# Kernel optimization log

Measured on AMD Instinct MI355X. Metric: run time of the kernel, lower is better.

Reference implementation:

```python
import jax, jax.numpy as jnp
import numpy as np
from jax import lax

B, S, DIMS, T, K = 4, 4096, 2048, 10, 2


def setup_inputs() -> dict:
    key = jax.random.key(0)
    ks = jax.random.split(key, 4)
    scale = 1.0 / np.sqrt(DIMS)
    x = jax.random.normal(ks[0], (B, S, DIMS), dtype=jnp.float32)
    W_cls = jax.random.normal(ks[1], (DIMS, T), dtype=jnp.float32) * scale
    W_sparse = jax.random.normal(ks[2], (DIMS, T), dtype=jnp.float32) * scale
    W_gates = jax.random.normal(ks[3], (DIMS, T), dtype=jnp.float32) * scale
    return {
        "x": x,
        "W_cls": W_cls, "b_cls": jnp.zeros((T,), jnp.float32),
        "W_sparse": W_sparse, "b_sparse": jnp.zeros((T,), jnp.float32),
        "W_gates": W_gates, "b_gates": jnp.zeros((T,), jnp.float32),
        "alpha": jnp.ones((1,), jnp.float32),
    }


def reference(x, W_cls, b_cls, W_sparse, b_sparse, W_gates, b_gates, alpha):
    # soft routing: softmax classifier over num_types
    soft_types = jax.nn.softmax(jnp.einsum("bsd,dt->bst", x, W_cls) + b_cls, axis=-1)
    # sparse routing: top-k over logits, softmax over the k kept logits,
    # scattered back into a dense [B,S,T] gate vector (zeros elsewhere)
    logits = jnp.einsum("bsd,dt->bst", x, W_sparse) + b_sparse
    top_v, top_i = lax.top_k(logits, K)                      # [B,S,K]
    sparse_g = jax.nn.softmax(top_v, axis=-1)                # [B,S,K]
    # scatter via one-hot (K and T are tiny)
    sparse_types = jnp.sum(jax.nn.one_hot(top_i, T, dtype=x.dtype) * sparse_g[..., None], axis=-2)  # [B,S,T]
    # per-type sigmoid gates: batched single matmul == stack of Linear(dims,1)+Sigmoid
    gates = jax.nn.sigmoid(jnp.einsum("bsd,dt->bst", x, W_gates) + b_gates)  # [B,S,T]
    a = jax.nn.sigmoid(alpha)                                # [1], broadcasts
    mixed_types = a * sparse_types + (1.0 - a) * soft_types  # [B,S,T]
    # original: gates stacked as [B,S,1,T], mixed unsqueezed to [B,S,1,T], sum over T -> [B,S,1]
    return jnp.sum(gates * mixed_types, axis=-1, keepdims=True)
```

## Files before the change

### kernel.cpp

```cpp
#include <hip/hip_runtime.h>
#include <math.h>
#include <stdint.h>


#define NROWS   16384
#define DIMS_   2048
#define TT      10
#define PIPE_D  3

typedef __attribute__((ext_vector_type(8))) short short8;
typedef __attribute__((ext_vector_type(4))) float f32x4;

__device__ __forceinline__ unsigned short bf16_rne(float f) {
    unsigned int u = __float_as_uint(f);
    unsigned int r = u + 0x7fffu + ((u >> 16) & 1u);
    return (unsigned short)(r >> 16);
}

__global__ __launch_bounds__(256)
void tgate_k0(const float* __restrict__ W_cls,
              const float* __restrict__ W_sparse,
              const float* __restrict__ W_gates,
              unsigned short* __restrict__ frag)
{
    int t = blockIdx.x * 256 + threadIdx.x;
    int K0   = t >> 7;
    int nt   = (t >> 6) & 1;
    int lane = t & 63;
    int n  = nt * 16 + (lane & 15);
    int kb = K0 * 32 + (lane >> 4) * 8;
    short8 hi, lo;
    #pragma unroll
    for (int j = 0; j < 8; ++j) {
        int k = kb + j;
        float w = 0.0f;
        if (n < 10)      w = W_cls[k * TT + n];
        else if (n < 20) w = W_sparse[k * TT + n - 10];
        else if (n < 30) w = W_gates[k * TT + n - 20];
        unsigned short h = bf16_rne(w);
        float back = __uint_as_float(((unsigned int)h) << 16);
        hi[j] = (short)h;
        lo[j] = (short)bf16_rne(w - back);
    }
    short8* fv = reinterpret_cast<short8*>(frag);
    fv[(K0 * 4 + nt * 2 + 0) * 64 + lane] = hi;
    fv[(K0 * 4 + nt * 2 + 1) * 64 + lane] = lo;
}

__global__ __launch_bounds__(256)
void tgate_k1(const float* __restrict__ x,
              const unsigned short* __restrict__ frag,
              const float* __restrict__ b_cls,
              const float* __restrict__ b_sparse,
              const float* __restrict__ b_gates,
              const float* __restrict__ alpha,
              float* __restrict__ out)
{
    __shared__ alignas(16) float red_lds[8 * 16 * 33 + 16 * 33];

    const int tid   = threadIdx.x;
    const int lane  = tid & 63;
    const int wv    = __builtin_amdgcn_readfirstlane(tid >> 6);
    const int row0  = blockIdx.x * 16;
    const int m     = lane & 15;
    const int quad  = lane >> 4;
    const int cbase = wv * 512;

    const short8* fv    = reinterpret_cast<const short8*>(frag);
    const short8* fbase = fv + (16 * wv * 4) * 64 + lane;
    const float*  xrow  = x + (size_t)(row0 + m) * DIMS_ + cbase + quad * 8;

    f32x4 acc[2][2];
    #pragma unroll
    for (int h = 0; h < 2; ++h) {
        acc[h][0] = (f32x4){0.f, 0.f, 0.f, 0.f};
        acc[h][1] = (f32x4){0.f, 0.f, 0.f, 0.f};
    }

    float4 xa[PIPE_D], xb[PIPE_D];
    short8 fh0[PIPE_D], fl0[PIPE_D], fh1[PIPE_D], fl1[PIPE_D];

    #pragma unroll
    for (int p = 0; p < PIPE_D; ++p) {
        fh0[p] = fbase[(p * 4 + 0) * 64];
        fl0[p] = fbase[(p * 4 + 1) * 64];
        fh1[p] = fbase[(p * 4 + 2) * 64];
        fl1[p] = fbase[(p * 4 + 3) * 64];
        xa[p]  = *reinterpret_cast<const float4*>(xrow + p * 32);
        xb[p]  = *reinterpret_cast<const float4*>(xrow + p * 32 + 4);
    }

    #pragma unroll
    for (int k = 0; k < 16; ++k) {
        const int sl = k % PIPE_D;
        const int h  = k >> 3;

        float f[8] = {xa[sl].x, xa[sl].y, xa[sl].z, xa[sl].w,
                      xb[sl].x, xb[sl].y, xb[sl].z, xb[sl].w};
        short8 ah, al;
        #pragma unroll
        for (int j = 0; j < 8; ++j) {
            unsigned short hh = bf16_rne(f[j]);
            float back = __uint_as_float(((unsigned int)hh) << 16);
            ah[j] = (short)hh;
            al[j] = (short)bf16_rne(f[j] - back);
        }
        short8 h0 = fh0[sl], l0 = fl0[sl], h1 = fh1[sl], l1 = fl1[sl];

        acc[h][0] = __builtin_amdgcn_mfma_f32_16x16x32_bf16(ah, h0, acc[h][0], 0, 0, 0);
        acc[h][0] = __builtin_amdgcn_mfma_f32_16x16x32_bf16(al, h0, acc[h][0], 0, 0, 0);
        acc[h][0] = __builtin_amdgcn_mfma_f32_16x16x32_bf16(ah, l0, acc[h][0], 0, 0, 0);
        acc[h][1] = __builtin_amdgcn_mfma_f32_16x16x32_bf16(ah, h1, acc[h][1], 0, 0, 0);
        acc[h][1] = __builtin_amdgcn_mfma_f32_16x16x32_bf16(al, h1, acc[h][1], 0, 0, 0);
        acc[h][1] = __builtin_amdgcn_mfma_f32_16x16x32_bf16(ah, l1, acc[h][1], 0, 0, 0);

        if (k + PIPE_D < 16) {
            const int kn = k + PIPE_D;
            fh0[sl] = fbase[(kn * 4 + 0) * 64];
            fl0[sl] = fbase[(kn * 4 + 1) * 64];
            fh1[sl] = fbase[(kn * 4 + 2) * 64];
            fl1[sl] = fbase[(kn * 4 + 3) * 64];
            xa[sl]  = *reinterpret_cast<const float4*>(xrow + kn * 32);
            xb[sl]  = *reinterpret_cast<const float4*>(xrow + kn * 32 + 4);
        }
    }

    float* red = red_lds;
    #pragma unroll
    for (int h = 0; h < 2; ++h) {
        int s = 2 * wv + h;
        #pragma unroll
        for (int r = 0; r < 4; ++r) {
            int row = quad * 4 + r;
            red[(s * 16 + row) * 33 + m]      = acc[h][0][r];
            red[(s * 16 + row) * 33 + m + 16] = acc[h][1][r];
        }
    }
    __syncthreads();

    float* fold = red + 8 * 16 * 33;
    #pragma unroll
    for (int u = 0; u < 2; ++u) {
        int i = tid * 2 + u;
        int row = i >> 5, j = i & 31;
        float a = 0.0f;
        #pragma unroll
        for (int s = 0; s < 8; ++s) a += red[(s * 16 + row) * 33 + j];
        fold[row * 33 + j] = a;
    }
    __syncthreads();

    if (tid < 16) {
        const float* l = &fold[tid * 33];
        float lc[TT], lsp[TT], g[TT];
        #pragma unroll
        for (int t = 0; t < TT; ++t) {
            lc[t]  = l[t]      + b_cls[t];
            lsp[t] = l[10 + t] + b_sparse[t];
            float lg = l[20 + t] + b_gates[t];
            g[t] = 1.0f / (1.0f + __expf(-lg));
        }
        float mm = lc[0];
        #pragma unroll
        for (int t = 1; t < TT; ++t) mm = fmaxf(mm, lc[t]);
        float esum = 0.0f, gdot = 0.0f;
        #pragma unroll
        for (int t = 0; t < TT; ++t) {
            float e = __expf(lc[t] - mm);
            esum += e;
            gdot = fmaf(g[t], e, gdot);
        }
        float v1 = lsp[0], v2 = -1e30f, gv1 = g[0], gv2 = 0.0f;
        #pragma unroll
        for (int t = 1; t < TT; ++t) {
            if (lsp[t] > v1)      { v2 = v1; gv2 = gv1; v1 = lsp[t]; gv1 = g[t]; }
            else if (lsp[t] > v2) { v2 = lsp[t]; gv2 = g[t]; }
        }
        float s1 = 1.0f / (1.0f + __expf(v2 - v1));
        float s2 = 1.0f - s1;
        float a  = 1.0f / (1.0f + __expf(-alpha[0]));
        float sparse_dot = fmaf(gv1, s1, gv2 * s2);
        out[row0 + tid] = fmaf(a, sparse_dot, (1.0f - a) * (gdot / esum));
    }
}

extern "C" void kernel_launch(void* const* d_in, const int* in_sizes, int n_in,
                              void* d_out, int out_size, void* d_ws, size_t ws_size,
                              hipStream_t stream) {
    const float* x        = (const float*)d_in[0];
    const float* W_cls    = (const float*)d_in[1];
    const float* b_cls    = (const float*)d_in[2];
    const float* W_sparse = (const float*)d_in[3];
    const float* b_sparse = (const float*)d_in[4];
    const float* W_gates  = (const float*)d_in[5];
    const float* b_gates  = (const float*)d_in[6];
    const float* alpha    = (const float*)d_in[7];
    float* out = (float*)d_out;

    unsigned short* frag = (unsigned short*)d_ws;

    tgate_k0<<<dim3(32), dim3(256), 0, stream>>>(W_cls, W_sparse, W_gates, frag);
    tgate_k1<<<dim3(NROWS / 16), dim3(256), 0, stream>>>(x, frag, b_cls, b_sparse,
                                                         b_gates, alpha, out);
}
```

Measured before the change: 210.9 us.

## Stage x tiles into LDS via direct global_load_lds in two half-spans

Replaces per-lane register prefetch of x rows with direct global-to-LDS loads (global_load_lds). Each wave stages a 16x256 span of x into its own LDS buffer, padded to a 260-float row stride, and refills it once at the midpoint. The weight-fragment prefetch depth is reduced to two slots. The aim is fully coalesced 1KB-per-row loads and lower VGPR pressure, at the cost of LDS traffic and a hard wait mid-loop that stalls before the second half is loaded. The LDS reuse for the reduction needs an added __syncthreads.

```diff
diff --git a/kernel.cpp b/kernel.cpp
--- a/kernel.cpp
+++ b/kernel.cpp
@@ -6,7 +6,6 @@
 #define NROWS   16384
 #define DIMS_   2048
 #define TT      10
-#define PIPE_D  3
 
 typedef __attribute__((ext_vector_type(8))) short short8;
 typedef __attribute__((ext_vector_type(4))) float f32x4;
@@ -47,6 +46,20 @@
     fv[(K0 * 4 + nt * 2 + 1) * 64 + lane] = lo;
 }
 
+__device__ __forceinline__ void stage_span(const float* __restrict__ x,
+                                           float* buf, int row0, int lane,
+                                           int colf0)
+{
+    #pragma unroll
+    for (int r = 0; r < 16; ++r) {
+        const float* gp = x + (size_t)(row0 + r) * DIMS_ + colf0 + lane * 4;
+        __builtin_amdgcn_global_load_lds(
+            (const __attribute__((address_space(1))) void*)gp,
+            (__attribute__((address_space(3))) void*)(buf + r * 260),
+            16, 0, 0);
+    }
+}
+
 __global__ __launch_bounds__(256)
 void tgate_k1(const float* __restrict__ x,
               const unsigned short* __restrict__ frag,
@@ -56,7 +69,7 @@
               const float* __restrict__ alpha,
               float* __restrict__ out)
 {
-    __shared__ alignas(16) float red_lds[8 * 16 * 33 + 16 * 33];
+    __shared__ alignas(16) float smem[4 * 4160];
 
     const int tid   = threadIdx.x;
     const int lane  = tid & 63;
@@ -66,9 +79,9 @@
     const int quad  = lane >> 4;
     const int cbase = wv * 512;
 
+    float* buf = smem + wv * 4160;
     const short8* fv    = reinterpret_cast<const short8*>(frag);
     const short8* fbase = fv + (16 * wv * 4) * 64 + lane;
-    const float*  xrow  = x + (size_t)(row0 + m) * DIMS_ + cbase + quad * 8;
 
     f32x4 acc[2][2];
     #pragma unroll
@@ -77,26 +90,35 @@
         acc[h][1] = (f32x4){0.f, 0.f, 0.f, 0.f};
     }
 
-    float4 xa[PIPE_D], xb[PIPE_D];
-    short8 fh0[PIPE_D], fl0[PIPE_D], fh1[PIPE_D], fl1[PIPE_D];
-
-    #pragma unroll
-    for (int p = 0; p < PIPE_D; ++p) {
-        fh0[p] = fbase[(p * 4 + 0) * 64];
-        fl0[p] = fbase[(p * 4 + 1) * 64];
-        fh1[p] = fbase[(p * 4 + 2) * 64];
-        fl1[p] = fbase[(p * 4 + 3) * 64];
-        xa[p]  = *reinterpret_cast<const float4*>(xrow + p * 32);
-        xb[p]  = *reinterpret_cast<const float4*>(xrow + p * 32 + 4);
-    }
+    stage_span(x, buf, row0, lane, cbase);
+    __builtin_amdgcn_sched_barrier(0);
+
+    short8 F[2][4];
+    #pragma unroll
+    for (int p = 0; p < 2; ++p) {
+        #pragma unroll
+        for (int j = 0; j < 4; ++j)
+            F[p][j] = fbase[(p * 4 + j) * 64];
+    }
+    __builtin_amdgcn_sched_barrier(0);
+
+    __builtin_amdgcn_s_waitcnt(0x0F78);
+    __builtin_amdgcn_sched_barrier(0);
 
     #pragma unroll
     for (int k = 0; k < 16; ++k) {
-        const int sl = k % PIPE_D;
-        const int h  = k >> 3;
-
-        float f[8] = {xa[sl].x, xa[sl].y, xa[sl].z, xa[sl].w,
-                      xb[sl].x, xb[sl].y, xb[sl].z, xb[sl].w};
+        if (k == 8) {
+            __builtin_amdgcn_s_waitcnt(0xC07F);
+            __builtin_amdgcn_sched_barrier(0);
+            stage_span(x, buf, row0, lane, cbase + 256);
+            __builtin_amdgcn_s_waitcnt(0x0F70);
+            __builtin_amdgcn_sched_barrier(0);
+        }
+        const int h = k >> 3;
+        const float* src = buf + m * 260 + (k & 7) * 32 + quad * 8;
+        float4 b0 = *reinterpret_cast<const float4*>(src);
+        float4 b1 = *reinterpret_cast<const float4*>(src + 4);
+        float f[8] = {b0.x, b0.y, b0.z, b0.w, b1.x, b1.y, b1.z, b1.w};
         short8 ah, al;
         #pragma unroll
         for (int j = 0; j < 8; ++j) {
@@ -105,7 +127,8 @@
             ah[j] = (short)hh;
             al[j] = (short)bf16_rne(f[j] - back);
         }
-        short8 h0 = fh0[sl], l0 = fl0[sl], h1 = fh1[sl], l1 = fl1[sl];
+        short8 h0 = F[k & 1][0], l0 = F[k & 1][1];
+        short8 h1 = F[k & 1][2], l1 = F[k & 1][3];
 
         acc[h][0] = __builtin_amdgcn_mfma_f32_16x16x32_bf16(ah, h0, acc[h][0], 0, 0, 0);
         acc[h][0] = __builtin_amdgcn_mfma_f32_16x16x32_bf16(al, h0, acc[h][0], 0, 0, 0);
@@ -114,18 +137,15 @@
         acc[h][1] = __builtin_amdgcn_mfma_f32_16x16x32_bf16(al, h1, acc[h][1], 0, 0, 0);
         acc[h][1] = __builtin_amdgcn_mfma_f32_16x16x32_bf16(ah, l1, acc[h][1], 0, 0, 0);
 
-        if (k + PIPE_D < 16) {
-            const int kn = k + PIPE_D;
-            fh0[sl] = fbase[(kn * 4 + 0) * 64];
-            fl0[sl] = fbase[(kn * 4 + 1) * 64];
-            fh1[sl] = fbase[(kn * 4 + 2) * 64];
-            fl1[sl] = fbase[(kn * 4 + 3) * 64];
-            xa[sl]  = *reinterpret_cast<const float4*>(xrow + kn * 32);
-            xb[sl]  = *reinterpret_cast<const float4*>(xrow + kn * 32 + 4);
-        }
-    }
-
-    float* red = red_lds;
+        if (k + 2 < 16) {
+            #pragma unroll
+            for (int j = 0; j < 4; ++j)
+                F[k & 1][j] = fbase[((k + 2) * 4 + j) * 64];
+        }
+    }
+
+    float* red = smem;
+    __syncthreads();
     #pragma unroll
     for (int h = 0; h < 2; ++h) {
         int s = 2 * wv + h;
```

Result: no change. 209.8 us (-0.5%).
